# Kernel optimization log

Measured on AMD Instinct MI355X. Metric: run time of the kernel, lower is better.

## Reference

```python
import jax, jax.numpy as jnp
import numpy as np

B, HP, WP = 4, 32, 32
T = HP * WP
C = 768            # n_embd
NH = 24            # n_head
HS = C // NH       # head_size == HEAD_SIZE == 32
E = HS             # TIME_MIX_EXTRA_DIM = HEAD_SIZE
D = 64             # TIME_DECAY_DIM


def setup_inputs() -> dict:
    key = jax.random.key(0)
    ks = jax.random.split(key, 24)
    small = lambda k, sh: jax.random.uniform(k, sh, jnp.float32, -1e-4, 1e-4)
    inp = {
        "x": jax.random.normal(ks[0], (B, T, C), jnp.float32),
        "time_maa_x": jax.random.uniform(ks[1], (1, 1, C), jnp.float32),
        "time_maa_w": jax.random.uniform(ks[2], (1, 1, C), jnp.float32),
        "time_maa_k": jax.random.uniform(ks[3], (1, 1, C), jnp.float32),
        "time_maa_v": jax.random.uniform(ks[4], (1, 1, C), jnp.float32),
        "time_maa_r": jax.random.uniform(ks[5], (1, 1, C), jnp.float32),
        "time_maa_g": jax.random.uniform(ks[6], (1, 1, C), jnp.float32),
        "time_maa_w1": small(ks[7], (C, 5 * E)),
        "time_maa_w2": small(ks[8], (5, E, C)),
        "time_decay": jnp.linspace(-6.0, -1.0, C, dtype=jnp.float32).reshape(1, 1, C),
        "time_decay_w1": small(ks[9], (C, D)),
        "time_decay_w2": small(ks[10], (D, C)),
        "time_faaaa": jax.random.uniform(ks[11], (NH, HS), jnp.float32, -0.1, 0.6),
        "W_r": jax.random.normal(ks[12], (C, C), jnp.float32) * 0.02,
        "W_k": jax.random.normal(ks[13], (C, C), jnp.float32) * 0.02,
        "W_v": jax.random.normal(ks[14], (C, C), jnp.float32) * 0.02,
        "W_g": jax.random.normal(ks[15], (C, C), jnp.float32) * 0.02,
        "W_o": jax.random.normal(ks[16], (C, C), jnp.float32) * 0.02,
        "ln_w": jnp.ones((C,), jnp.float32),
        "ln_b": jnp.zeros((C,), jnp.float32),
        "Hp": HP,
        "Wp": WP,
    }
    return inp


def q_shift(x, H, W):
    """groups_q_shift with K=1, gamma=1/4: quarter-channel 4-direction spatial shift, zero-padded."""
    Bs, Ts, Cs = x.shape
    g = x.reshape(Bs, H, W, Cs)
    c4 = Cs // 4
    a, b, c, d = g[..., :c4], g[..., c4:2 * c4], g[..., 2 * c4:3 * c4], g[..., 3 * c4:]
    a = jnp.pad(a[:, :, :-1], ((0, 0), (0, 0), (1, 0), (0, 0)))  # shift +W (right)
    b = jnp.pad(b[:, :, 1:], ((0, 0), (0, 0), (0, 1), (0, 0)))   # shift -W (left)
    c = jnp.pad(c[:, :-1], ((0, 0), (1, 0), (0, 0), (0, 0)))     # shift +H (down)
    d = jnp.pad(d[:, 1:], ((0, 0), (0, 1), (0, 0), (0, 0)))      # shift -H (up)
    return jnp.concatenate([a, b, c, d], axis=-1).reshape(Bs, Ts, Cs)


def wkv6(r, k, v, w, u):
    """RWKV6 WKV scan. r,k,v,w: (B,T,C); u: (NH,HS). decay = exp(-exp(w))."""
    Bs, Ts, Cs = r.shape
    rh = r.reshape(Bs, Ts, NH, HS)
    kh = k.reshape(Bs, Ts, NH, HS)
    vh = v.reshape(Bs, Ts, NH, HS)
    dh = jnp.exp(-jnp.exp(w)).reshape(Bs, Ts, NH, HS)

    def step(s, ins):
        rt, kt, vt, dt = ins                                   # each (B,NH,HS)
        kv = kt[..., :, None] * vt[..., None, :]               # (B,NH,HS,HS)
        y = jnp.einsum('bhj,bhji->bhi', rt, s + u[None, :, :, None] * kv)
        s = dt[..., :, None] * s + kv
        return s, y

    xs = (rh.transpose(1, 0, 2, 3), kh.transpose(1, 0, 2, 3),
          vh.transpose(1, 0, 2, 3), dh.transpose(1, 0, 2, 3))
    s0 = jnp.zeros((Bs, NH, HS, HS), r.dtype)
    _, ys = jax.lax.scan(step, s0, xs)                          # (T,B,NH,HS)
    return ys.transpose(1, 0, 2, 3).reshape(Bs, Ts, Cs)


def reference(x, time_maa_x, time_maa_w, time_maa_k, time_maa_v, time_maa_r,
              time_maa_g, time_maa_w1, time_maa_w2, time_decay, time_decay_w1,
              time_decay_w2, time_faaaa, W_r, W_k, W_v, W_g, W_o, ln_w, ln_b,
              Hp, Wp):
    Bs, Ts, Cs = x.shape
    xx = q_shift(x, Hp, Wp) - x                                 # token shift delta
    xxx = x + xx * time_maa_x
    xxx = jnp.tanh(xxx @ time_maa_w1).reshape(Bs, Ts, 5, E)
    mix = jnp.einsum('btke,kec->kbtc', xxx, time_maa_w2)        # (5,B,T,C)
    mw, mk, mv, mr, mg = mix[0], mix[1], mix[2], mix[3], mix[4]

    xw = x + xx * (time_maa_w + mw)
    xk = x + xx * (time_maa_k + mk)
    xv = x + xx * (time_maa_v + mv)
    xr = x + xx * (time_maa_r + mr)
    xg = x + xx * (time_maa_g + mg)

    r = xr @ W_r
    k = xk @ W_k
    v = xv @ W_v
    g = jax.nn.silu(xg @ W_g)

    ww = jnp.tanh(xw @ time_decay_w1) @ time_decay_w2
    w = time_decay + ww                                         # data-dependent log-decay

    y = wkv6(r, k, v, w, time_faaaa)

    # ln_x (LayerNorm over channels)
    mu = y.mean(-1, keepdims=True)
    var = ((y - mu) ** 2).mean(-1, keepdims=True)
    yn = (y - mu) / jnp.sqrt(var + 1e-5) * ln_w + ln_b

    return (yn * g) @ W_o
```

## Files before the change

kernel.cpp:

```cpp
#include <hip/hip_runtime.h>
#include <math.h>

#define BB   4
#define TT   1024
#define CC   768
#define NH_  24
#define HS_  32
#define NBH  (BB * NH_)
#define NCH  16
#define CL   64

static constexpr size_t SZ = (size_t)BB * TT * CC;

typedef __attribute__((ext_vector_type(8))) __bf16 bf16x8;
typedef __attribute__((ext_vector_type(4))) float  f32x4;

__device__ __forceinline__ unsigned short f2bf(float f) {
    unsigned u = __float_as_uint(f);
    unsigned r = (u + 0x7FFFu + ((u >> 16) & 1u)) >> 16;
    return (unsigned short)r;
}
__device__ __forceinline__ float bf2f(unsigned short h) {
    return __uint_as_float(((unsigned)h) << 16);
}

__device__ __forceinline__ void gload16(const unsigned short* g, unsigned short* l)
{
    __builtin_amdgcn_global_load_lds(
        (const __attribute__((address_space(1))) void*)(g),
        (__attribute__((address_space(3))) void*)(l),
        16, 0, 0);
}

__device__ __forceinline__ int xcd_swz(int wg, int nwg)
{
    return (wg & 7) * (nwg >> 3) + (wg >> 3);
}

struct TDesc { const float* src; unsigned short* dst; int R, C; };
struct TArgs { TDesc d[8]; };

__global__ __launch_bounds__(256) void transpose_cast(TArgs a)
{
    __shared__ float tile[32][33];
    TDesc t = a.d[blockIdx.z];
    const int tx0 = blockIdx.x * 32, ty0 = blockIdx.y * 32;
    if (tx0 >= t.C || ty0 >= t.R) return;
    const int tx = threadIdx.x & 31, ty = threadIdx.x >> 5;
    #pragma unroll
    for (int dy = 0; dy < 4; ++dy) {
        int rr = ty0 + ty + dy * 8, cc = tx0 + tx;
        tile[ty + dy * 8][tx] = (rr < t.R && cc < t.C) ? t.src[(size_t)rr * t.C + cc] : 0.f;
    }
    __syncthreads();
    #pragma unroll
    for (int dy = 0; dy < 4; ++dy) {
        int cc = tx0 + ty + dy * 8, rr = ty0 + tx;
        if (cc < t.C && rr < t.R)
            t.dst[(size_t)cc * t.R + rr] = f2bf(tile[tx][ty + dy * 8]);
    }
}

__global__ __launch_bounds__(192) void w2fill(const float* __restrict__ w2,
                                              unsigned short* __restrict__ W2t)
{
    const int n = blockIdx.x;
    const int e = threadIdx.x;
    if (e >= 160) return;
    const int kk = n / 768;
    const int c  = n - kk * 768;
    unsigned short val = 0;
    if ((e >> 5) == kk) val = f2bf(w2[(size_t)e * 768 + c]);
    W2t[(size_t)n * 160 + e] = val;
}

__global__ __launch_bounds__(256) void shift_kernel(
    const float* __restrict__ x, const float* __restrict__ maa_x,
    float* __restrict__ xxO, unsigned short* __restrict__ xxxO)
{
    const int tok = blockIdx.x;
    const int t   = tok & (TT - 1);
    const int hh  = t >> 5;
    const int wp  = t & 31;
    const int tid = threadIdx.x;
    const float* xrow = x + (size_t)tok * CC;
    for (int c = tid; c < CC; c += 256) {
        float xc = xrow[c];
        float sh;
        if (c < 192)      sh = (wp > 0)  ? xrow[c - CC]      : 0.f;
        else if (c < 384) sh = (wp < 31) ? xrow[c + CC]      : 0.f;
        else if (c < 576) sh = (hh > 0)  ? xrow[c - 32 * CC] : 0.f;
        else              sh = (hh < 31) ? xrow[c + 32 * CC] : 0.f;
        float xxv = sh - xc;
        size_t o = (size_t)tok * CC + c;
        xxO[o]  = xxv;
        xxxO[o] = f2bf(fmaf(xxv, maa_x[c], xc));
    }
}

template<int KDIM, class Epi>
__device__ __forceinline__ void gemm_core(const unsigned short* __restrict__ A,
                                          const unsigned short* __restrict__ W,
                                          int N, const Epi& epi)
{
    __shared__ __align__(16) unsigned short As[64][40];
    __shared__ __align__(16) unsigned short Bs[64][40];

    const int tid  = threadIdx.x;
    const int lane = tid & 63;
    const int wv   = tid >> 6;
    const int wm   = (wv >> 1) * 32, wn = (wv & 1) * 32;
    const int m0   = blockIdx.y * 64, n0 = blockIdx.x * 64;
    const int srow = tid >> 2, scb = (tid & 3) * 8;
    const int l15  = lane & 15, kb8 = (lane >> 4) * 8;

    f32x4 acc[2][2];
    #pragma unroll
    for (int a = 0; a < 2; ++a)
        #pragma unroll
        for (int b = 0; b < 2; ++b)
            #pragma unroll
            for (int e = 0; e < 4; ++e) acc[a][b][e] = 0.f;

    const unsigned short* aP = A + (size_t)(m0 + srow) * KDIM + scb;
    const unsigned short* bP = W + (size_t)(n0 + srow) * KDIM + scb;
    const bool bvalid = (n0 + srow) < N;

    for (int k0 = 0; k0 < KDIM; k0 += 32) {
        uint4 av = *(const uint4*)(aP + k0);
        uint4 bw = make_uint4(0u, 0u, 0u, 0u);
        if (bvalid) bw = *(const uint4*)(bP + k0);
        *(uint4*)&As[srow][scb] = av;
        *(uint4*)&Bs[srow][scb] = bw;
        __syncthreads();

        bf16x8 a0 = *(const bf16x8*)&As[wm + l15][kb8];
        bf16x8 a1 = *(const bf16x8*)&As[wm + 16 + l15][kb8];
        bf16x8 b0 = *(const bf16x8*)&Bs[wn + l15][kb8];
        bf16x8 b1 = *(const bf16x8*)&Bs[wn + 16 + l15][kb8];
        acc[0][0] = __builtin_amdgcn_mfma_f32_16x16x32_bf16(a0, b0, acc[0][0], 0, 0, 0);
        acc[0][1] = __builtin_amdgcn_mfma_f32_16x16x32_bf16(a0, b1, acc[0][1], 0, 0, 0);
        acc[1][0] = __builtin_amdgcn_mfma_f32_16x16x32_bf16(a1, b0, acc[1][0], 0, 0, 0);
        acc[1][1] = __builtin_amdgcn_mfma_f32_16x16x32_bf16(a1, b1, acc[1][1], 0, 0, 0);
        __syncthreads();
    }

    const int rb_ = m0 + wm + (lane >> 4) * 4;
    #pragma unroll
    for (int mi = 0; mi < 2; ++mi)
        #pragma unroll
        for (int ni = 0; ni < 2; ++ni) {
            int col = n0 + wn + ni * 16 + l15;
            if (col < N) {
                #pragma unroll
                for (int j = 0; j < 4; ++j)
                    epi(rb_ + mi * 16 + j, col, acc[mi][ni][j]);
            }
        }
}

template<int KDIM, class Epi>
__device__ __forceinline__ void gemm_core128(const unsigned short* __restrict__ A,
                                             const unsigned short* __restrict__ W,
                                             int N, int m0, int n0, const Epi& epi)
{
    __shared__ __align__(16) unsigned short As[128][32];
    __shared__ __align__(16) unsigned short Bs[128][32];

    const int tid  = threadIdx.x;
    const int lane = tid & 63;
    const int wv   = tid >> 6;
    const int wm   = (wv >> 1) * 64, wn = (wv & 1) * 64;
    const int l15  = lane & 15, kb8 = (lane >> 4) * 8, rb4 = (lane >> 4) * 4;
    const int sr   = tid >> 2, sq = (tid & 3) * 8;

    f32x4 acc[4][4];
    #pragma unroll
    for (int a = 0; a < 4; ++a)
        #pragma unroll
        for (int b = 0; b < 4; ++b)
            #pragma unroll
            for (int e = 0; e < 4; ++e) acc[a][b][e] = 0.f;

    const unsigned short* aP  = A + (size_t)(m0 + sr) * KDIM + sq;
    const unsigned short* aP2 = A + (size_t)(m0 + 64 + sr) * KDIM + sq;
    const unsigned short* bP  = W + (size_t)(n0 + sr) * KDIM + sq;
    const unsigned short* bP2 = W + (size_t)(n0 + 64 + sr) * KDIM + sq;
    unsigned short* asD  = &As[sr][sq];
    unsigned short* asD2 = &As[64 + sr][sq];
    unsigned short* bsD  = &Bs[sr][sq];
    unsigned short* bsD2 = &Bs[64 + sr][sq];

    for (int k0 = 0; k0 < KDIM; k0 += 32) {
        gload16(aP + k0,  asD);
        gload16(aP2 + k0, asD2);
        gload16(bP + k0,  bsD);
        gload16(bP2 + k0, bsD2);
        __syncthreads();

        bf16x8 af[4], bfr[4];
        #pragma unroll
        for (int mi = 0; mi < 4; ++mi)
            af[mi] = *(const bf16x8*)&As[wm + mi * 16 + l15][kb8];
        #pragma unroll
        for (int ni = 0; ni < 4; ++ni)
            bfr[ni] = *(const bf16x8*)&Bs[wn + ni * 16 + l15][kb8];
        #pragma unroll
        for (int mi = 0; mi < 4; ++mi)
            #pragma unroll
            for (int ni = 0; ni < 4; ++ni)
                acc[mi][ni] = __builtin_amdgcn_mfma_f32_16x16x32_bf16(af[mi], bfr[ni], acc[mi][ni], 0, 0, 0);
        __syncthreads();
    }

    const int rbase = m0 + wm + rb4;
    #pragma unroll
    for (int mi = 0; mi < 4; ++mi)
        #pragma unroll
        for (int ni = 0; ni < 4; ++ni) {
            int col = n0 + wn + ni * 16 + l15;
            if (col < N) {
                #pragma unroll
                for (int j = 0; j < 4; ++j)
                    epi(rbase + mi * 16 + j, col, acc[mi][ni][j]);
            }
        }
}

struct EpiTanh {
    unsigned short* O; int ldo;
    __device__ void operator()(int r, int c, float v) const {
        O[(size_t)r * ldo + c] = f2bf(tanhf(v));
    }
};
struct EpiF32 {
    float* O;
    __device__ void operator()(int r, int c, float v) const {
        O[(size_t)r * 768 + c] = v;
    }
};
struct EpiDec {
    const float* td; float* O;
    __device__ void operator()(int r, int c, float v) const {
        O[(size_t)r * 768 + c] = expf(-expf(td[c] + v));
    }
};
struct EpiMix {
    const float* px; const float* pxx;
    const float* maa[5];
    unsigned short* outs[5];
    __device__ void operator()(int r, int c, float v) const {
        int kk = c / 768;
        int cc = c - kk * 768;
        size_t o = (size_t)r * 768 + cc;
        outs[kk][o] = f2bf(fmaf(pxx[o], maa[kk][cc] + v, px[o]));
    }
};
struct EpiRKVG {
    unsigned short* O; bool silu;
    __device__ void operator()(int r, int c, float v) const {
        if (silu) v = v / (1.f + expf(-v));
        O[(size_t)r * 768 + c] = f2bf(v);
    }
};

template<int KDIM, class Epi>
__global__ __launch_bounds__(256) void gemm_one(const unsigned short* __restrict__ A,
                                                const unsigned short* __restrict__ W,
                                                int N, Epi epi)
{
    gemm_core<KDIM>(A, W, N, epi);
}

template<int KDIM, int NB, class Epi>
__global__ __launch_bounds__(256) void gemm_one128(const unsigned short* __restrict__ A,
                                                   const unsigned short* __restrict__ W,
                                                   int N, Epi epi)
{
    const int idx = xcd_swz(blockIdx.x, gridDim.x);
    const int m0 = (idx / NB) * 128, n0 = (idx % NB) * 128;
    gemm_core128<KDIM>(A, W, N, m0, n0, epi);
}

struct QuadArgs {
    const unsigned short* A[4];
    const unsigned short* W[4];
    unsigned short* O[4];
};
__global__ __launch_bounds__(256) void gemm_quad768(QuadArgs q)
{
    const int idx = xcd_swz(blockIdx.x, 768);
    const int z = idx / 192;
    const int rz = idx - z * 192;
    const int m0 = (rz / 6) * 128, n0 = (rz % 6) * 128;
    EpiRKVG e{q.O[z], z == 3};
    gemm_core128<768>(q.A[z], q.W[z], 768, m0, n0, e);
}

__global__ __launch_bounds__(256) void wkv_local(
    const unsigned short* __restrict__ r, const unsigned short* __restrict__ k,
    const unsigned short* __restrict__ v, const float* __restrict__ dec,
    const float* __restrict__ u, float* __restrict__ y,
    unsigned short* __restrict__ rsb, float* __restrict__ kvt,
    float* __restrict__ dcv)
{
    __shared__ __align__(16) unsigned short rwL[64][40], kwL[64][40];
    __shared__ __align__(16) unsigned short vT0[32][40], vT1[32][40];
    __shared__ __align__(16) unsigned short ksT0[32][40], ksT1[32][40];
    __shared__ __align__(16) unsigned short PL0[64][40], PL1[64][40];
    __shared__ float AL[65][32];
    __shared__ float segprod[8][32];
    __shared__ float dpart[64][4];
    __shared__ float diagL[64];
    __shared__ float uL[32];

    const int c   = blockIdx.x;
    const int bh  = blockIdx.y;
    const int b = bh / NH_, h = bh % NH_;
    const int tid  = threadIdx.x;
    const int lane = tid & 63;
    const int wv   = tid >> 6;
    const int l15  = lane & 15;
    const int kb8  = (lane >> 4) * 8;
    const int rb4  = (lane >> 4) * 4;
    const int tc   = c * CL;

    const size_t base0 = ((size_t)b * TT) * CC + (size_t)h * HS_;

    if (tid < 32) uL[tid] = u[h * HS_ + tid];

    const int lrow = tid >> 2, lq = (tid & 3) * 8;
    const int cj = tid & 31, cseg = tid >> 5;

    {
        size_t gp = base0 + (size_t)(tc + lrow) * CC + lq;
        uint4 rv = *(const uint4*)(r + gp);
        uint4 kv = *(const uint4*)(k + gp);
        uint4 vv = *(const uint4*)(v + gp);
        *(uint4*)&rwL[lrow][lq] = rv;
        *(uint4*)&kwL[lrow][lq] = kv;
        const unsigned short* vp = (const unsigned short*)&vv;
        if (lrow < 32) {
            #pragma unroll
            for (int e = 0; e < 8; ++e) vT0[lq + e][lrow] = vp[e];
        } else {
            #pragma unroll
            for (int e = 0; e < 8; ++e) vT1[lq + e][lrow - 32] = vp[e];
        }
    }
    float dv[8];
    #pragma unroll
    for (int q = 0; q < 8; ++q)
        dv[q] = dec[base0 + (size_t)(tc + cseg * 8 + q) * CC + cj];
    {
        float lp = dv[0];
        #pragma unroll
        for (int q = 1; q < 8; ++q) lp *= dv[q];
        segprod[cseg][cj] = lp;
    }
    __syncthreads();

    {
        const int ptau = tid >> 2, pp = tid & 3;
        float acc = 0.f;
        #pragma unroll
        for (int e = 0; e < 8; ++e) {
            int j = pp * 8 + e;
            acc += bf2f(rwL[ptau][j]) * uL[j] * bf2f(kwL[ptau][j]);
        }
        dpart[ptau][pp] = acc;
    }
    {
        float pre = 1.f;
        #pragma unroll
        for (int s = 0; s < 7; ++s) if (s < cseg) pre *= segprod[s][cj];
        float run = pre;
        #pragma unroll
        for (int q = 0; q < 8; ++q) {
            AL[cseg * 8 + q][cj] = run;
            run *= dv[q];
        }
        if (cseg == 7) AL[64][cj] = run;
    }
    __syncthreads();

    if (tid < 64)
        diagL[tid] = dpart[tid][0] + dpart[tid][1] + dpart[tid][2] + dpart[tid][3];
    if (tid < 32)
        dcv[((size_t)bh * NCH + c) * 32 + tid] = AL[64][tid];

    #pragma unroll
    for (int q = 0; q < 8; ++q) {
        int tau = cseg * 8 + q;
        float a  = AL[tau][cj];
        float ia = 1.f / AL[tau + 1][cj];
        unsigned short rs = f2bf(bf2f(rwL[tau][cj]) * a);
        unsigned short ks = f2bf(bf2f(kwL[tau][cj]) * ia);
        rwL[tau][cj] = rs;
        kwL[tau][cj] = ks;
        if (tau < 32) ksT0[cj][tau] = ks; else ksT1[cj][tau - 32] = ks;
    }
    __syncthreads();

    {
        const int wm = (wv >> 1) * 32, wn = (wv & 1) * 32;
        bf16x8 a0 = *(const bf16x8*)&rwL[wm + l15][kb8];
        bf16x8 a1 = *(const bf16x8*)&rwL[wm + 16 + l15][kb8];
        bf16x8 b0 = *(const bf16x8*)&kwL[wn + l15][kb8];
        bf16x8 b1 = *(const bf16x8*)&kwL[wn + 16 + l15][kb8];
        f32x4 qf[2][2];
        #pragma unroll
        for (int mi = 0; mi < 2; ++mi)
            #pragma unroll
            for (int ni = 0; ni < 2; ++ni)
                #pragma unroll
                for (int e = 0; e < 4; ++e) qf[mi][ni][e] = 0.f;
        qf[0][0] = __builtin_amdgcn_mfma_f32_16x16x32_bf16(a0, b0, qf[0][0], 0, 0, 0);
        qf[0][1] = __builtin_amdgcn_mfma_f32_16x16x32_bf16(a0, b1, qf[0][1], 0, 0, 0);
        qf[1][0] = __builtin_amdgcn_mfma_f32_16x16x32_bf16(a1, b0, qf[1][0], 0, 0, 0);
        qf[1][1] = __builtin_amdgcn_mfma_f32_16x16x32_bf16(a1, b1, qf[1][1], 0, 0, 0);
        #pragma unroll
        for (int mi = 0; mi < 2; ++mi)
            #pragma unroll
            for (int ni = 0; ni < 2; ++ni) {
                const int col = wn + ni * 16 + l15;
                #pragma unroll
                for (int jj = 0; jj < 4; ++jj) {
                    const int row = wm + mi * 16 + rb4 + jj;
                    float val = (col < row) ? qf[mi][ni][jj]
                              : ((col == row) ? diagL[row] : 0.f);
                    unsigned short bvv = f2bf(val);
                    if (col < 32) PL0[row][col] = bvv;
                    else          PL1[row][col - 32] = bvv;
                }
            }
    }
    __syncthreads();

    *(uint4*)(rsb + base0 + (size_t)(tc + lrow) * CC + lq) = *(const uint4*)&rwL[lrow][lq];

    {
        const int mr = wv * 16;
        bf16x8 pa0 = *(const bf16x8*)&PL0[mr + l15][kb8];
        bf16x8 pa1 = *(const bf16x8*)&PL1[mr + l15][kb8];
        #pragma unroll
        for (int ni = 0; ni < 2; ++ni) {
            bf16x8 bv0 = *(const bf16x8*)&vT0[ni * 16 + l15][kb8];
            bf16x8 bv1 = *(const bf16x8*)&vT1[ni * 16 + l15][kb8];
            f32x4 acc;
            #pragma unroll
            for (int e = 0; e < 4; ++e) acc[e] = 0.f;
            acc = __builtin_amdgcn_mfma_f32_16x16x32_bf16(pa0, bv0, acc, 0, 0, 0);
            acc = __builtin_amdgcn_mfma_f32_16x16x32_bf16(pa1, bv1, acc, 0, 0, 0);
            #pragma unroll
            for (int jj = 0; jj < 4; ++jj)
                y[base0 + (size_t)(tc + mr + rb4 + jj) * CC + ni * 16 + l15] = acc[jj];
        }
    }

    {
        const int mi_ = (wv >> 1) * 16, nj = (wv & 1) * 16;
        bf16x8 av0 = *(const bf16x8*)&vT0[mi_ + l15][kb8];
        bf16x8 av1 = *(const bf16x8*)&vT1[mi_ + l15][kb8];
        bf16x8 bk0 = *(const bf16x8*)&ksT0[nj + l15][kb8];
        bf16x8 bk1 = *(const bf16x8*)&ksT1[nj + l15][kb8];
        f32x4 acc;
        #pragma unroll
        for (int e = 0; e < 4; ++e) acc[e] = 0.f;
        acc = __builtin_amdgcn_mfma_f32_16x16x32_bf16(av0, bk0, acc, 0, 0, 0);
        acc = __builtin_amdgcn_mfma_f32_16x16x32_bf16(av1, bk1, acc, 0, 0, 0);
        const int j = nj + l15;
        const size_t sb = ((size_t)bh * NCH + c) << 10;
        #pragma unroll
        for (int jj = 0; jj < 4; ++jj)
            kvt[sb + (size_t)(mi_ + rb4 + jj) * 32 + j] = acc[jj];
    }
}

__global__ __launch_bounds__(256) void wkv_carry(
    const float* __restrict__ kvt, const float* __restrict__ dcv,
    unsigned short* __restrict__ spv)
{
    const int bh = blockIdx.x;
    const int tid = threadIdx.x;
    const int e0 = tid << 2;
    const int j0 = e0 & 31;
    float s0 = 0.f, s1 = 0.f, s2 = 0.f, s3 = 0.f;
    #pragma unroll
    for (int c = 0; c < NCH; ++c) {
        const size_t sb = (size_t)bh * NCH + c;
        float4 kv = *(const float4*)(kvt + (sb << 10) + e0);
        float4 d4 = *(const float4*)(dcv + sb * 32 + j0);
        s0 = d4.x * (s0 + kv.x);
        s1 = d4.y * (s1 + kv.y);
        s2 = d4.z * (s2 + kv.z);
        s3 = d4.w * (s3 + kv.w);
        if (c < NCH - 1) {
            unsigned lo = (unsigned)f2bf(s0) | ((unsigned)f2bf(s1) << 16);
            unsigned hi = (unsigned)f2bf(s2) | ((unsigned)f2bf(s3) << 16);
            *(uint2*)(spv + ((sb + 1) << 10) + e0) = make_uint2(lo, hi);
        }
    }
}

__global__ __launch_bounds__(256) void wkv_stadd(
    const unsigned short* __restrict__ rsb, const unsigned short* __restrict__ spv,
    float* __restrict__ y)
{
    __shared__ __align__(16) unsigned short rsL[64][40];
    __shared__ __align__(16) unsigned short STb[32][40];

    const int c  = blockIdx.x + 1;
    const int bh = blockIdx.y;
    const int b = bh / NH_, h = bh % NH_;
    const int tid = threadIdx.x, lane = tid & 63, wv = tid >> 6;
    const int l15 = lane & 15, kb8 = (lane >> 4) * 8, rb4 = (lane >> 4) * 4;
    const int tc = c * CL;
    const size_t base0 = ((size_t)b * TT) * CC + (size_t)h * HS_;
    const int lrow = tid >> 2, lq = (tid & 3) * 8;

    *(uint4*)&rsL[lrow][lq] = *(const uint4*)(rsb + base0 + (size_t)(tc + lrow) * CC + lq);
    if (tid < 128) {
        int row = tid >> 2, q = (tid & 3) * 8;
        *(uint4*)&STb[row][q] =
            *(const uint4*)(spv + (((size_t)bh * NCH + c) << 10) + (size_t)row * 32 + q);
    }
    __syncthreads();

    const int mr = wv * 16;
    bf16x8 ra = *(const bf16x8*)&rsL[mr + l15][kb8];
    #pragma unroll
    for (int ni = 0; ni < 2; ++ni) {
        bf16x8 bs = *(const bf16x8*)&STb[ni * 16 + l15][kb8];
        f32x4 acc;
        #pragma unroll
        for (int e = 0; e < 4; ++e) acc[e] = 0.f;
        acc = __builtin_amdgcn_mfma_f32_16x16x32_bf16(ra, bs, acc, 0, 0, 0);
        #pragma unroll
        for (int jj = 0; jj < 4; ++jj) {
            size_t gp = base0 + (size_t)(tc + mr + rb4 + jj) * CC + ni * 16 + l15;
            y[gp] += acc[jj];
        }
    }
}

__global__ __launch_bounds__(256) void ln_gate(
    const float* __restrict__ y, const unsigned short* __restrict__ g,
    const float* __restrict__ lnw, const float* __restrict__ lnb,
    unsigned short* __restrict__ z)
{
    __shared__ float sy[CC];
    __shared__ float rbuf[8];
    __shared__ float stats[2];

    const int row = blockIdx.x, tid = threadIdx.x;
    const float* yr = y + (size_t)row * CC;

    float s1 = 0.f, s2 = 0.f;
    #pragma unroll
    for (int q = 0; q < 3; ++q) {
        int c = tid + q * 256;
        float vv = yr[c];
        sy[c] = vv;
        s1 += vv;
        s2 += vv * vv;
    }
    #pragma unroll
    for (int off = 32; off > 0; off >>= 1) {
        s1 += __shfl_down(s1, off);
        s2 += __shfl_down(s2, off);
    }
    const int wid = tid >> 6;
    if ((tid & 63) == 0) { rbuf[wid] = s1; rbuf[4 + wid] = s2; }
    __syncthreads();
    if (tid == 0) {
        float S1 = rbuf[0] + rbuf[1] + rbuf[2] + rbuf[3];
        float S2 = rbuf[4] + rbuf[5] + rbuf[6] + rbuf[7];
        float mu = S1 / (float)CC;
        float var = S2 / (float)CC - mu * mu;
        stats[0] = mu;
        stats[1] = rsqrtf(var + 1e-5f);
    }
    __syncthreads();
    const float mu = stats[0], rstd = stats[1];
    const unsigned short* gr = g + (size_t)row * CC;
    unsigned short* zr = z + (size_t)row * CC;
    #pragma unroll
    for (int q = 0; q < 3; ++q) {
        int c = tid + q * 256;
        zr[c] = f2bf(fmaf((sy[c] - mu) * rstd, lnw[c], lnb[c]) * bf2f(gr[c]));
    }
}

extern "C" void kernel_launch(void* const* d_in, const int* in_sizes, int n_in,
                              void* d_out, int out_size, void* d_ws, size_t ws_size,
                              hipStream_t stream)
{
    const float* x      = (const float*)d_in[0];
    const float* maa_x  = (const float*)d_in[1];
    const float* maa_w  = (const float*)d_in[2];
    const float* maa_k  = (const float*)d_in[3];
    const float* maa_v  = (const float*)d_in[4];
    const float* maa_r  = (const float*)d_in[5];
    const float* maa_g  = (const float*)d_in[6];
    const float* w1     = (const float*)d_in[7];
    const float* w2     = (const float*)d_in[8];
    const float* tdec   = (const float*)d_in[9];
    const float* tdw1   = (const float*)d_in[10];
    const float* tdw2   = (const float*)d_in[11];
    const float* faaaa  = (const float*)d_in[12];
    const float* Wr     = (const float*)d_in[13];
    const float* Wk     = (const float*)d_in[14];
    const float* Wv     = (const float*)d_in[15];
    const float* Wg     = (const float*)d_in[16];
    const float* Wo     = (const float*)d_in[17];
    const float* lnw    = (const float*)d_in[18];
    const float* lnb    = (const float*)d_in[19];

    char* base = (char*)d_ws;
    size_t off = 0;
    auto alloc = [&](size_t bytes) -> char* {
        char* p = base + off;
        off = (off + bytes + 255) & ~(size_t)255;
        return p;
    };

    float*          xx   = (float*)alloc(SZ * 4);
    float*          decb = (float*)alloc(SZ * 4);
    unsigned short* xxx  = (unsigned short*)alloc(SZ * 2);
    unsigned short* xw   = (unsigned short*)alloc(SZ * 2);
    unsigned short* xk   = (unsigned short*)alloc(SZ * 2);
    unsigned short* xv   = (unsigned short*)alloc(SZ * 2);
    unsigned short* xr   = (unsigned short*)alloc(SZ * 2);
    unsigned short* xg   = (unsigned short*)alloc(SZ * 2);
    unsigned short* rb   = (unsigned short*)alloc(SZ * 2);
    unsigned short* kb   = (unsigned short*)alloc(SZ * 2);
    unsigned short* vb   = (unsigned short*)alloc(SZ * 2);
    unsigned short* gb   = (unsigned short*)alloc(SZ * 2);
    unsigned short* t5   = (unsigned short*)alloc((size_t)4096 * 160 * 2);
    unsigned short* d1   = (unsigned short*)alloc((size_t)4096 * 64 * 2);
    unsigned short* w1t  = (unsigned short*)alloc((size_t)160 * 768 * 2);
    unsigned short* w2t  = (unsigned short*)alloc((size_t)3840 * 160 * 2);
    unsigned short* wrt  = (unsigned short*)alloc((size_t)768 * 768 * 2);
    unsigned short* wkt  = (unsigned short*)alloc((size_t)768 * 768 * 2);
    unsigned short* wvt  = (unsigned short*)alloc((size_t)768 * 768 * 2);
    unsigned short* wgt  = (unsigned short*)alloc((size_t)768 * 768 * 2);
    unsigned short* wot  = (unsigned short*)alloc((size_t)768 * 768 * 2);
    unsigned short* td1t = (unsigned short*)alloc((size_t)64 * 768 * 2);
    unsigned short* td2t = (unsigned short*)alloc((size_t)768 * 64 * 2);

    float*          y    = xx;
    unsigned short* z    = xxx;
    unsigned short* rsb  = xr;
    float*          kvtb = (float*)xk;
    unsigned short* spvb = xv;
    float*          dcb  = (float*)xg;

    TArgs ta = {{
        { w1,   w1t,  768, 160 },
        { Wr,   wrt,  768, 768 },
        { Wk,   wkt,  768, 768 },
        { Wv,   wvt,  768, 768 },
        { Wg,   wgt,  768, 768 },
        { Wo,   wot,  768, 768 },
        { tdw1, td1t, 768, 64  },
        { tdw2, td2t, 64,  768 },
    }};
    transpose_cast<<<dim3(24, 24, 8), 256, 0, stream>>>(ta);
    w2fill<<<3840, 192, 0, stream>>>(w2, w2t);

    shift_kernel<<<BB * TT, 256, 0, stream>>>(x, maa_x, xx, xxx);

    gemm_one<768, EpiTanh><<<dim3(3, 64), 256, 0, stream>>>(xxx, w1t, 160, EpiTanh{t5, 160});

    EpiMix em{ x, xx,
               { maa_w, maa_k, maa_v, maa_r, maa_g },
               { xw, xk, xv, xr, xg } };
    gemm_one128<160, 30, EpiMix><<<960, 256, 0, stream>>>(t5, w2t, 3840, em);

    gemm_one<768, EpiTanh><<<dim3(1, 64), 256, 0, stream>>>(xw, td1t, 64, EpiTanh{d1, 64});

    gemm_one<64, EpiDec><<<dim3(12, 64), 256, 0, stream>>>(d1, td2t, 768, EpiDec{tdec, decb});

    QuadArgs qa = {{ xr, xk, xv, xg }, { wrt, wkt, wvt, wgt }, { rb, kb, vb, gb }};
    gemm_quad768<<<768, 256, 0, stream>>>(qa);

    wkv_local<<<dim3(NCH, NBH), 256, 0, stream>>>(rb, kb, vb, decb, faaaa, y, rsb, kvtb, dcb);
    wkv_carry<<<NBH, 256, 0, stream>>>(kvtb, dcb, spvb);
    wkv_stadd<<<dim3(NCH - 1, NBH), 256, 0, stream>>>(rsb, spvb, y);

    ln_gate<<<BB * TT, 256, 0, stream>>>(y, gb, lnw, lnb, z);

    gemm_one128<768, 6, EpiF32><<<192, 256, 0, stream>>>(z, wot, 768, EpiF32{(float*)d_out});
}
```

Baseline: 267.2 us.

## Double-buffer shared tiles in 128 GEMM core and fuse decay LoRA GEMMs

The 128x128 GEMM core now uses two shared-memory buffers, so the next K-slice is loaded while MFMAs run on the current one, and each iteration needs one barrier instead of two. The two decay-LoRA GEMMs (tanh(xw@W1) then exp(-exp(td+..@W2))) are merged into one kernel that keeps the 64x64 tanh intermediate in LDS, which removes a launch and the global round trip through d1. The tradeoffs are double the LDS use in the GEMM core, which may cut occupancy, and a fused decay kernel that runs on only 64 blocks with 768-column serial loops, which may leave many CUs idle.

```diff
diff --git a/kernel.cpp b/kernel.cpp
--- a/kernel.cpp
+++ b/kernel.cpp
@@ -164,8 +164,8 @@
                                              const unsigned short* __restrict__ W,
                                              int N, int m0, int n0, const Epi& epi)
 {
-    __shared__ __align__(16) unsigned short As[128][32];
-    __shared__ __align__(16) unsigned short Bs[128][32];
+    __shared__ __align__(16) unsigned short As[2][128][32];
+    __shared__ __align__(16) unsigned short Bs[2][128][32];
 
     const int tid  = threadIdx.x;
     const int lane = tid & 63;
@@ -186,31 +186,40 @@
     const unsigned short* aP2 = A + (size_t)(m0 + 64 + sr) * KDIM + sq;
     const unsigned short* bP  = W + (size_t)(n0 + sr) * KDIM + sq;
     const unsigned short* bP2 = W + (size_t)(n0 + 64 + sr) * KDIM + sq;
-    unsigned short* asD  = &As[sr][sq];
-    unsigned short* asD2 = &As[64 + sr][sq];
-    unsigned short* bsD  = &Bs[sr][sq];
-    unsigned short* bsD2 = &Bs[64 + sr][sq];
-
-    for (int k0 = 0; k0 < KDIM; k0 += 32) {
-        gload16(aP + k0,  asD);
-        gload16(aP2 + k0, asD2);
-        gload16(bP + k0,  bsD);
-        gload16(bP2 + k0, bsD2);
-        __syncthreads();
+
+    constexpr int NT = KDIM / 32;
+
+    gload16(aP,  &As[0][sr][sq]);
+    gload16(aP2, &As[0][64 + sr][sq]);
+    gload16(bP,  &Bs[0][sr][sq]);
+    gload16(bP2, &Bs[0][64 + sr][sq]);
+    __syncthreads();
+
+    int cur = 0;
+    for (int t = 0; t < NT; ++t) {
+        if (t + 1 < NT) {
+            const int k0 = (t + 1) * 32;
+            gload16(aP + k0,  &As[cur ^ 1][sr][sq]);
+            gload16(aP2 + k0, &As[cur ^ 1][64 + sr][sq]);
+            gload16(bP + k0,  &Bs[cur ^ 1][sr][sq]);
+            gload16(bP2 + k0, &Bs[cur ^ 1][64 + sr][sq]);
+        }
 
         bf16x8 af[4], bfr[4];
         #pragma unroll
         for (int mi = 0; mi < 4; ++mi)
-            af[mi] = *(const bf16x8*)&As[wm + mi * 16 + l15][kb8];
+            af[mi] = *(const bf16x8*)&As[cur][wm + mi * 16 + l15][kb8];
         #pragma unroll
         for (int ni = 0; ni < 4; ++ni)
-            bfr[ni] = *(const bf16x8*)&Bs[wn + ni * 16 + l15][kb8];
+            bfr[ni] = *(const bf16x8*)&Bs[cur][wn + ni * 16 + l15][kb8];
         #pragma unroll
         for (int mi = 0; mi < 4; ++mi)
             #pragma unroll
             for (int ni = 0; ni < 4; ++ni)
                 acc[mi][ni] = __builtin_amdgcn_mfma_f32_16x16x32_bf16(af[mi], bfr[ni], acc[mi][ni], 0, 0, 0);
+
         __syncthreads();
+        cur ^= 1;
     }
 
     const int rbase = m0 + wm + rb4;
@@ -237,12 +246,6 @@
     float* O;
     __device__ void operator()(int r, int c, float v) const {
         O[(size_t)r * 768 + c] = v;
-    }
-};
-struct EpiDec {
-    const float* td; float* O;
-    __device__ void operator()(int r, int c, float v) const {
-        O[(size_t)r * 768 + c] = expf(-expf(td[c] + v));
     }
 };
 struct EpiMix {
@@ -295,6 +298,90 @@
     const int m0 = (rz / 6) * 128, n0 = (rz % 6) * 128;
     EpiRKVG e{q.O[z], z == 3};
     gemm_core128<768>(q.A[z], q.W[z], 768, m0, n0, e);
+}
+
+__global__ __launch_bounds__(256) void decay_fused(
+    const unsigned short* __restrict__ xw, const unsigned short* __restrict__ td1t,
+    const unsigned short* __restrict__ td2t, const float* __restrict__ td,
+    float* __restrict__ decO)
+{
+    __shared__ __align__(16) unsigned short As[64][40];
+    __shared__ __align__(16) unsigned short Bs[64][40];
+    __shared__ __align__(16) unsigned short Tl[64][72];
+    __shared__ __align__(16) unsigned short B2[64][72];
+
+    const int tid  = threadIdx.x;
+    const int lane = tid & 63;
+    const int wv   = tid >> 6;
+    const int wm   = (wv >> 1) * 32, wn = (wv & 1) * 32;
+    const int l15  = lane & 15, kb8 = (lane >> 4) * 8, rb4 = (lane >> 4) * 4;
+    const int m0   = blockIdx.x * 64;
+    const int srow = tid >> 2, scb = (tid & 3) * 8;
+
+    f32x4 acc[2][2];
+    #pragma unroll
+    for (int a = 0; a < 2; ++a)
+        #pragma unroll
+        for (int b = 0; b < 2; ++b)
+            #pragma unroll
+            for (int e = 0; e < 4; ++e) acc[a][b][e] = 0.f;
+
+    const unsigned short* aP = xw + (size_t)(m0 + srow) * 768 + scb;
+    const unsigned short* bP = td1t + (size_t)srow * 768 + scb;
+    for (int k0 = 0; k0 < 768; k0 += 32) {
+        *(uint4*)&As[srow][scb] = *(const uint4*)(aP + k0);
+        *(uint4*)&Bs[srow][scb] = *(const uint4*)(bP + k0);
+        __syncthreads();
+        bf16x8 a0 = *(const bf16x8*)&As[wm + l15][kb8];
+        bf16x8 a1 = *(const bf16x8*)&As[wm + 16 + l15][kb8];
+        bf16x8 b0 = *(const bf16x8*)&Bs[wn + l15][kb8];
+        bf16x8 b1 = *(const bf16x8*)&Bs[wn + 16 + l15][kb8];
+        acc[0][0] = __builtin_amdgcn_mfma_f32_16x16x32_bf16(a0, b0, acc[0][0], 0, 0, 0);
+        acc[0][1] = __builtin_amdgcn_mfma_f32_16x16x32_bf16(a0, b1, acc[0][1], 0, 0, 0);
+        acc[1][0] = __builtin_amdgcn_mfma_f32_16x16x32_bf16(a1, b0, acc[1][0], 0, 0, 0);
+        acc[1][1] = __builtin_amdgcn_mfma_f32_16x16x32_bf16(a1, b1, acc[1][1], 0, 0, 0);
+        __syncthreads();
+    }
+    #pragma unroll
+    for (int mi = 0; mi < 2; ++mi)
+        #pragma unroll
+        for (int ni = 0; ni < 2; ++ni) {
+            const int col = wn + ni * 16 + l15;
+            #pragma unroll
+            for (int jj = 0; jj < 4; ++jj)
+                Tl[wm + mi * 16 + rb4 + jj][col] = f2bf(tanhf(acc[mi][ni][jj]));
+        }
+    __syncthreads();
+
+    const int sr2 = tid >> 2, sq2 = (tid & 3) * 16;
+    for (int n0 = 0; n0 < 768; n0 += 64) {
+        *(uint4*)&B2[sr2][sq2]     = *(const uint4*)(td2t + (size_t)(n0 + sr2) * 64 + sq2);
+        *(uint4*)&B2[sr2][sq2 + 8] = *(const uint4*)(td2t + (size_t)(n0 + sr2) * 64 + sq2 + 8);
+        __syncthreads();
+
+        #pragma unroll
+        for (int mi = 0; mi < 2; ++mi) {
+            bf16x8 aL = *(const bf16x8*)&Tl[wm + mi * 16 + l15][kb8];
+            bf16x8 aH = *(const bf16x8*)&Tl[wm + mi * 16 + l15][32 + kb8];
+            #pragma unroll
+            for (int ni = 0; ni < 2; ++ni) {
+                bf16x8 bL = *(const bf16x8*)&B2[wn + ni * 16 + l15][kb8];
+                bf16x8 bH = *(const bf16x8*)&B2[wn + ni * 16 + l15][32 + kb8];
+                f32x4 a2;
+                #pragma unroll
+                for (int e = 0; e < 4; ++e) a2[e] = 0.f;
+                a2 = __builtin_amdgcn_mfma_f32_16x16x32_bf16(aL, bL, a2, 0, 0, 0);
+                a2 = __builtin_amdgcn_mfma_f32_16x16x32_bf16(aH, bH, a2, 0, 0, 0);
+                const int col = n0 + wn + ni * 16 + l15;
+                #pragma unroll
+                for (int jj = 0; jj < 4; ++jj) {
+                    const int row = m0 + wm + mi * 16 + rb4 + jj;
+                    decO[(size_t)row * 768 + col] = expf(-expf(td[col] + a2[jj]));
+                }
+            }
+        }
+        __syncthreads();
+    }
 }
 
 __global__ __launch_bounds__(256) void wkv_local(
@@ -648,6 +735,7 @@
     unsigned short* wot  = (unsigned short*)alloc((size_t)768 * 768 * 2);
     unsigned short* td1t = (unsigned short*)alloc((size_t)64 * 768 * 2);
     unsigned short* td2t = (unsigned short*)alloc((size_t)768 * 64 * 2);
+    (void)d1;
 
     float*          y    = xx;
     unsigned short* z    = xxx;
@@ -678,9 +766,7 @@
                { xw, xk, xv, xr, xg } };
     gemm_one128<160, 30, EpiMix><<<960, 256, 0, stream>>>(t5, w2t, 3840, em);
 
-    gemm_one<768, EpiTanh><<<dim3(1, 64), 256, 0, stream>>>(xw, td1t, 64, EpiTanh{d1, 64});
-
-    gemm_one<64, EpiDec><<<dim3(12, 64), 256, 0, stream>>>(d1, td2t, 768, EpiDec{tdec, decb});
+    decay_fused<<<64, 256, 0, stream>>>(xw, td1t, td2t, tdec, decb);
 
     QuadArgs qa = {{ xr, xk, xv, xg }, { wrt, wkt, wvt, wgt }, { rb, kb, vb, gb }};
     gemm_quad768<<<768, 256, 0, stream>>>(qa);
```

Result: slower. 290.4 us (+8.7%).
